# Kernel optimization log

Hardware: AMD Instinct MI355X
Metric: run time of the kernel (lower is better)

## Reference

```python
import jax, jax.numpy as jnp
import numpy as np

NUM_EMBEDDINGS = 1024
DIM = 256
COMMIT = 0.25


def setup_inputs() -> dict:
    key = jax.random.key(0)
    k_inp, k_emb = jax.random.split(key)
    inp = jax.random.normal(k_inp, (64, 1024, DIM), dtype=jnp.float32)
    # emb.weight.data.uniform_(-1/num_embeddings, 1/num_embeddings)
    emb = jax.random.uniform(
        k_emb, (NUM_EMBEDDINGS, DIM), dtype=jnp.float32,
        minval=-1.0 / NUM_EMBEDDINGS, maxval=1.0 / NUM_EMBEDDINGS)
    return {"inp": inp, "emb": emb}


def reference(inp, emb):
    flat = inp.reshape(-1, DIM)                       # [N, D]
    d = (jnp.sum(flat * flat, axis=1, keepdims=True)
         + jnp.sum(emb * emb, axis=1)
         - 2.0 * flat @ emb.T)
    idx = jnp.argmin(d, axis=1)                       # [N]
    # gather instead of one-hot matmul (same math)
    quant = emb[idx].reshape(inp.shape)               # [B, T, D]
    codebook_loss = jnp.mean((jax.lax.stop_gradient(quant) - inp) ** 2)
    commit_loss = jnp.mean((quant - jax.lax.stop_gradient(inp)) ** 2)
    loss = codebook_loss + COMMIT * commit_loss
    st = inp + jax.lax.stop_gradient(quant - inp)     # straight-through
    return st, loss, idx
```

## Files before the change

kernel.cpp:

```cpp
#include <hip/hip_runtime.h>
#include <math.h>

#define D 256
#define K 1024
#define NR 65536
#define ST_SIZE (NR * D)
#define LOSS_OFF ST_SIZE
#define IDX_OFF (ST_SIZE + 1)
#define BM 128
#define TPB 512
#define NRND 32
#define NBLK (NR / BM)
#define MARGIN 2e-3f
#define CAND_CAP 3072

typedef short bf16x8 __attribute__((ext_vector_type(8)));
typedef float f32x4 __attribute__((ext_vector_type(4)));

#define GLDS(g, s) __builtin_amdgcn_global_load_lds( \
    (const __attribute__((address_space(1))) unsigned int*)(g), \
    (__attribute__((address_space(3))) unsigned int*)(s), 16, 0, 0)

__device__ __forceinline__ unsigned f2bf(float f) {
    unsigned u = __float_as_uint(f);
    return (u + 0x7FFFu + ((u >> 16) & 1u)) >> 16;
}
__device__ __forceinline__ uint4 packB(float4 a, float4 b) {
    uint4 w;
    w.x = f2bf(-2.f * a.x) | (f2bf(-2.f * a.y) << 16);
    w.y = f2bf(-2.f * a.z) | (f2bf(-2.f * a.w) << 16);
    w.z = f2bf(-2.f * b.x) | (f2bf(-2.f * b.y) << 16);
    w.w = f2bf(-2.f * b.z) | (f2bf(-2.f * b.w) << 16);
    return w;
}

__device__ __forceinline__ float sq_nf(float x) {
    float s = x * x;
    asm volatile("" : "+v"(s));
    return s;
}
template <typename F>
__device__ __forceinline__ float np_sumsq256(F ld) {
    float tot[2];
    #pragma unroll
    for (int h = 0; h < 2; ++h) {
        const int base = h * 128;
        float r[8];
        #pragma unroll
        for (int j = 0; j < 8; ++j) r[j] = sq_nf(ld(base + j));
        for (int i = 8; i < 128; i += 8) {
            #pragma unroll
            for (int j = 0; j < 8; ++j) r[j] += sq_nf(ld(base + i + j));
        }
        tot[h] = ((r[0] + r[1]) + (r[2] + r[3])) + ((r[4] + r[5]) + (r[6] + r[7]));
    }
    return tot[0] + tot[1];
}

__global__ void prep_kernel(const float* __restrict__ emb,
                            unsigned short* __restrict__ pb,
                            float* __restrict__ se) {
    if (blockIdx.x < 128) {
        const int c  = blockIdx.x * 256 + threadIdx.x;
        const int ct = c >> 9;
        const int r  = c & 511;
        const int kb = r >> 6, l = r & 63;
        const float* srcp = emb + (size_t)(ct * 16 + (l & 15)) * D
                                + kb * 32 + (l >> 4) * 8;
        const float4* s4 = (const float4*)srcp;
        ((uint4*)pb)[c] = packB(s4[0], s4[1]);
    } else {
        const int k = (blockIdx.x - 128) * 256 + threadIdx.x;
        const float* row = emb + (size_t)k * D;
        se[k] = np_sumsq256([&](int i) { return row[i]; });
    }
}

__global__ __attribute__((amdgpu_waves_per_eu(2, 4))) __launch_bounds__(TPB)
void vq_main(const float* __restrict__ inp, const float* __restrict__ emb,
             const unsigned short* __restrict__ pb, const float* __restrict__ se,
             float* __restrict__ out, double* __restrict__ lsum) {
    __shared__ __align__(16) unsigned short Bt[2][8192];
    __shared__ float sx_s[BM];
    __shared__ float rfin[BM];
    __shared__ unsigned cand[CAND_CAP];
    __shared__ float candsc[CAND_CAP];
    __shared__ unsigned bestd[BM];
    __shared__ unsigned bestc[BM];
    __shared__ int ncand;

    const int t   = threadIdx.x;
    const int ws  = t >> 6;
    const int l   = t & 63;
    const int c16 = l & 15;
    const int g4  = l >> 4;
    const int r0  = blockIdx.x * BM;

    if (t < BM) { bestd[t] = 0xFFFFFFFFu; bestc[t] = 0xFFFFFFFFu; }
    if (t == 0) ncand = 0;

    bf16x8 afr[8];
    {
        const float* xrow = inp + (size_t)(r0 + ws * 16 + c16) * D;
        #pragma unroll
        for (int kb = 0; kb < 8; ++kb) {
            const float4* p4 = (const float4*)(xrow + kb * 32 + g4 * 8);
            float4 a = p4[0], b = p4[1];
            bf16x8 v;
            v[0] = (short)f2bf(a.x); v[1] = (short)f2bf(a.y);
            v[2] = (short)f2bf(a.z); v[3] = (short)f2bf(a.w);
            v[4] = (short)f2bf(b.x); v[5] = (short)f2bf(b.y);
            v[6] = (short)f2bf(b.z); v[7] = (short)f2bf(b.w);
            afr[kb] = v;
        }
    }

    {
        const int slot = t & 15, grp = t >> 4;
        const int j = slot & 7, h = slot >> 3;
        #pragma unroll
        for (int p = 0; p < 4; ++p) {
            const int row = p * 32 + grp;
            const float* base = inp + (size_t)(r0 + row) * D + h * 128 + j;
            float s = sq_nf(base[0]);
            #pragma unroll
            for (int i = 1; i < 16; ++i) s += sq_nf(base[i * 8]);
            #pragma unroll
            for (int m = 1; m <= 8; m <<= 1) s += __shfl_xor(s, m);
            if (slot == 0) sx_s[row] = s;
        }
    }

    float rmin[4];
    #pragma unroll
    for (int i = 0; i < 4; ++i) rmin[i] = INFINITY;

    const uint4* srcv = (const uint4*)pb;

    auto stage = [&](int buf, int cr) {
        const uint4* g = srcv + (size_t)cr * 1024;
        #pragma unroll
        for (int q = 0; q < 2; ++q) {
            char* lbase = (char*)&Bt[buf][0] + (q * 512 + ws * 64) * 16;
            GLDS(g + q * TPB + t, lbase);
        }
    };

    stage(0, 0);
    int cur = 0;
    for (int cr = 0; cr < NRND; ++cr) {
        __syncthreads();
        if (cr + 1 < NRND) stage(cur ^ 1, cr + 1);
        const bf16x8* bch = (const bf16x8*)&Bt[cur][0];
        f32x4 a0e, a0o, a1e, a1o;
        {
            const float sev0 = se[(cr * 2 + 0) * 16 + c16];
            const float sev1 = se[(cr * 2 + 1) * 16 + c16];
            #pragma unroll
            for (int i = 0; i < 4; ++i) { a0e[i] = sev0; a0o[i] = 0.f; a1e[i] = sev1; a1o[i] = 0.f; }
        }
        #pragma unroll
        for (int kb = 0; kb < 8; kb += 2) {
            a0e = __builtin_amdgcn_mfma_f32_16x16x32_bf16(afr[kb],     bch[kb * 64 + l],             a0e, 0, 0, 0);
            a1e = __builtin_amdgcn_mfma_f32_16x16x32_bf16(afr[kb],     bch[512 + kb * 64 + l],       a1e, 0, 0, 0);
            a0o = __builtin_amdgcn_mfma_f32_16x16x32_bf16(afr[kb + 1], bch[(kb + 1) * 64 + l],       a0o, 0, 0, 0);
            a1o = __builtin_amdgcn_mfma_f32_16x16x32_bf16(afr[kb + 1], bch[512 + (kb + 1) * 64 + l], a1o, 0, 0, 0);
        }
        float sc0[4], sc1[4];
        #pragma unroll
        for (int i = 0; i < 4; ++i) { sc0[i] = a0e[i] + a0o[i]; sc1[i] = a1e[i] + a1o[i]; }

        #pragma unroll
        for (int i = 0; i < 4; ++i) rmin[i] = fminf(rmin[i], fminf(sc0[i], sc1[i]));
        if ((cr & 1) == 0) {
            #pragma unroll
            for (int i = 0; i < 4; ++i) {
                #pragma unroll
                for (int m = 1; m <= 8; m <<= 1)
                    rmin[i] = fminf(rmin[i], __shfl_xor(rmin[i], m));
            }
        }
        #pragma unroll
        for (int i = 0; i < 4; ++i) {
            const int row_local = ws * 16 + g4 * 4 + i;
            if (sc0[i] <= rmin[i] + MARGIN) {
                const int p = atomicAdd(&ncand, 1);
                if (p < CAND_CAP) {
                    cand[p]   = ((unsigned)row_local << 10) | (unsigned)((cr * 2) * 16 + c16);
                    candsc[p] = sc0[i];
                }
            }
            if (sc1[i] <= rmin[i] + MARGIN) {
                const int p = atomicAdd(&ncand, 1);
                if (p < CAND_CAP) {
                    cand[p]   = ((unsigned)row_local << 10) | (unsigned)((cr * 2 + 1) * 16 + c16);
                    candsc[p] = sc1[i];
                }
            }
        }
        cur ^= 1;
    }
    #pragma unroll
    for (int i = 0; i < 4; ++i) {
        #pragma unroll
        for (int m = 1; m <= 8; m <<= 1)
            rmin[i] = fminf(rmin[i], __shfl_xor(rmin[i], m));
    }
    if (c16 == 0) {
        #pragma unroll
        for (int i = 0; i < 4; ++i)
            rfin[ws * 16 + g4 * 4 + i] = rmin[i];
    }
    __syncthreads();

    int n = ncand; if (n > CAND_CAP) n = CAND_CAP;
    {
        const int qw = l >> 4, lq = l & 15;
        for (int ci = ws * 4 + qw; ci < n; ci += 32) {
            const unsigned uc = cand[ci];
            const int row_local = uc >> 10, code = uc & 1023;
            const float sc = candsc[ci];
            if (sc <= rfin[row_local] + MARGIN) {
                const float4* xp = (const float4*)(inp + (size_t)(r0 + row_local) * D) + lq * 4;
                const float4* ep = (const float4*)(emb + (size_t)code * D) + lq * 4;
                float p = 0.f;
                #pragma unroll
                for (int q = 0; q < 4; ++q) {
                    float4 x = xp[q], e = ep[q];
                    p = fmaf(x.x, e.x, p);
                    p = fmaf(x.y, e.y, p);
                    p = fmaf(x.z, e.z, p);
                    p = fmaf(x.w, e.w, p);
                }
                #pragma unroll
                for (int m = 1; m <= 8; m <<= 1) p += __shfl_xor(p, m);
                const float tv = sx_s[row_local] + se[code];
                const float d  = fmaf(-2.f, p, tv);
                if (lq == 0) {
                    candsc[ci] = d;
                    atomicMin(&bestd[row_local], __float_as_uint(d));
                }
            } else if (lq == 0) {
                candsc[ci] = INFINITY;
            }
        }
    }
    __syncthreads();
    for (int ci = t; ci < n; ci += TPB) {
        const unsigned uc = cand[ci];
        if (__float_as_uint(candsc[ci]) == bestd[uc >> 10])
            atomicMin(&bestc[uc >> 10], uc & 1023u);
    }
    __syncthreads();
    if (t < BM) out[IDX_OFF + r0 + t] = (float)bestc[t];

    {
        float4* out4 = (float4*)(out + (size_t)r0 * D);
        const float4* emb4 = (const float4*)emb;
        #pragma unroll
        for (int i = 0; i < (BM * D) / (4 * TPB); ++i) {
            const int e = i * TPB + t;
            out4[e] = emb4[((size_t)bestc[e >> 6] << 6) + (e & 63)];
        }
    }

    if (t < 64) {
        double s = (double)__uint_as_float(bestd[t]) + (double)__uint_as_float(bestd[t + 64]);
        #pragma unroll
        for (int m = 1; m < 64; m <<= 1) s += __shfl_xor(s, m);
        if (t == 0) lsum[blockIdx.x] = s;
    }
}

__global__ void fin_kernel(const double* __restrict__ lsum, float* __restrict__ out) {
    const int l = threadIdx.x;
    double s = 0.0;
    #pragma unroll
    for (int i = 0; i < NBLK / 64; ++i) s += lsum[l * (NBLK / 64) + i];
    #pragma unroll
    for (int m = 1; m < 64; m <<= 1) s += __shfl_xor(s, m);
    if (l == 0) out[LOSS_OFF] = (float)(1.25 * s / (double)ST_SIZE);
}

extern "C" void kernel_launch(void* const* d_in, const int* in_sizes, int n_in,
                              void* d_out, int out_size, void* d_ws, size_t ws_size,
                              hipStream_t stream) {
    const float* inp = (const float*)d_in[0];
    const float* emb = (const float*)d_in[1];
    float* out = (float*)d_out;
    unsigned short* pb = (unsigned short*)d_ws;
    float*  se_ws      = (float*)((char*)d_ws + 524288);
    double* lsum       = (double*)((char*)d_ws + 528384);

    prep_kernel<<<132, 256, 0, stream>>>(emb, pb, se_ws);
    vq_main<<<NBLK, TPB, 0, stream>>>(inp, emb, pb, se_ws, out, lsum);
    fin_kernel<<<1, 64, 0, stream>>>(lsum, out);
}
```

Measured before the change: 142.1 us.

## Double block size and split codebook halves across wave pairs per row group

Raises threads per block to 1024 so each 16-row group is handled by two waves that each scan half of the codebook, rather than one wave scanning all of it. Running minima per row are shared between the two waves through LDS atomicMin on order-preserving float keys, and that shared value is also used to prune candidates during the scan. The goal is more waves in flight to hide MFMA and LDS latency, and fewer candidate pushes. In exchange it adds atomics and barriers over more threads, and the larger block can raise register pressure or lower occupancy.

```diff
diff --git a/kernel.cpp b/kernel.cpp
--- a/kernel.cpp
+++ b/kernel.cpp
@@ -8,7 +8,7 @@
 #define LOSS_OFF ST_SIZE
 #define IDX_OFF (ST_SIZE + 1)
 #define BM 128
-#define TPB 512
+#define TPB 1024
 #define NRND 32
 #define NBLK (NR / BM)
 #define MARGIN 2e-3f
@@ -32,6 +32,15 @@
     w.z = f2bf(-2.f * b.x) | (f2bf(-2.f * b.y) << 16);
     w.w = f2bf(-2.f * b.z) | (f2bf(-2.f * b.w) << 16);
     return w;
+}
+
+__device__ __forceinline__ unsigned fkey(float f) {
+    unsigned b = __float_as_uint(f);
+    return (b & 0x80000000u) ? ~b : (b | 0x80000000u);
+}
+__device__ __forceinline__ float finv(unsigned u) {
+    unsigned b = (u & 0x80000000u) ? (u ^ 0x80000000u) : ~u;
+    return __uint_as_float(b);
 }
 
 __device__ __forceinline__ float sq_nf(float x) {
@@ -76,13 +85,13 @@
     }
 }
 
-__global__ __attribute__((amdgpu_waves_per_eu(2, 4))) __launch_bounds__(TPB)
+__global__ __attribute__((amdgpu_waves_per_eu(2, 8))) __launch_bounds__(TPB)
 void vq_main(const float* __restrict__ inp, const float* __restrict__ emb,
              const unsigned short* __restrict__ pb, const float* __restrict__ se,
              float* __restrict__ out, double* __restrict__ lsum) {
     __shared__ __align__(16) unsigned short Bt[2][8192];
     __shared__ float sx_s[BM];
-    __shared__ float rfin[BM];
+    __shared__ unsigned rminsh[BM];
     __shared__ unsigned cand[CAND_CAP];
     __shared__ float candsc[CAND_CAP];
     __shared__ unsigned bestd[BM];
@@ -94,14 +103,16 @@
     const int l   = t & 63;
     const int c16 = l & 15;
     const int g4  = l >> 4;
+    const int rg  = ws >> 1;
+    const int ch  = ws & 1;
     const int r0  = blockIdx.x * BM;
 
-    if (t < BM) { bestd[t] = 0xFFFFFFFFu; bestc[t] = 0xFFFFFFFFu; }
+    if (t < BM) { bestd[t] = 0xFFFFFFFFu; bestc[t] = 0xFFFFFFFFu; rminsh[t] = 0xFFFFFFFFu; }
     if (t == 0) ncand = 0;
 
     bf16x8 afr[8];
     {
-        const float* xrow = inp + (size_t)(r0 + ws * 16 + c16) * D;
+        const float* xrow = inp + (size_t)(r0 + rg * 16 + c16) * D;
         #pragma unroll
         for (int kb = 0; kb < 8; ++kb) {
             const float4* p4 = (const float4*)(xrow + kb * 32 + g4 * 8);
@@ -119,8 +130,8 @@
         const int slot = t & 15, grp = t >> 4;
         const int j = slot & 7, h = slot >> 3;
         #pragma unroll
-        for (int p = 0; p < 4; ++p) {
-            const int row = p * 32 + grp;
+        for (int p = 0; p < 2; ++p) {
+            const int row = p * 64 + grp;
             const float* base = inp + (size_t)(r0 + row) * D + h * 128 + j;
             float s = sq_nf(base[0]);
             #pragma unroll
@@ -138,12 +149,10 @@
     const uint4* srcv = (const uint4*)pb;
 
     auto stage = [&](int buf, int cr) {
-        const uint4* g = srcv + (size_t)cr * 1024;
-        #pragma unroll
-        for (int q = 0; q < 2; ++q) {
-            char* lbase = (char*)&Bt[buf][0] + (q * 512 + ws * 64) * 16;
-            GLDS(g + q * TPB + t, lbase);
-        }
+        const uint4* g = srcv + ((t < 512) ? ((size_t)cr * 512 + t)
+                                           : ((size_t)(32 + cr) * 512 + (t - 512)));
+        char* lbase = (char*)&Bt[buf][0] + ws * 1024;
+        GLDS(g, lbase);
     };
 
     stage(0, 0);
@@ -151,27 +160,25 @@
     for (int cr = 0; cr < NRND; ++cr) {
         __syncthreads();
         if (cr + 1 < NRND) stage(cur ^ 1, cr + 1);
-        const bf16x8* bch = (const bf16x8*)&Bt[cur][0];
-        f32x4 a0e, a0o, a1e, a1o;
+        const bf16x8* bch = (const bf16x8*)&Bt[cur][ch * 4096];
+        const int ct = ch * 32 + cr;
+        f32x4 aE, aO;
         {
-            const float sev0 = se[(cr * 2 + 0) * 16 + c16];
-            const float sev1 = se[(cr * 2 + 1) * 16 + c16];
-            #pragma unroll
-            for (int i = 0; i < 4; ++i) { a0e[i] = sev0; a0o[i] = 0.f; a1e[i] = sev1; a1o[i] = 0.f; }
+            const float sev = se[ct * 16 + c16];
+            #pragma unroll
+            for (int i = 0; i < 4; ++i) { aE[i] = sev; aO[i] = 0.f; }
         }
         #pragma unroll
         for (int kb = 0; kb < 8; kb += 2) {
-            a0e = __builtin_amdgcn_mfma_f32_16x16x32_bf16(afr[kb],     bch[kb * 64 + l],             a0e, 0, 0, 0);
-            a1e = __builtin_amdgcn_mfma_f32_16x16x32_bf16(afr[kb],     bch[512 + kb * 64 + l],       a1e, 0, 0, 0);
-            a0o = __builtin_amdgcn_mfma_f32_16x16x32_bf16(afr[kb + 1], bch[(kb + 1) * 64 + l],       a0o, 0, 0, 0);
-            a1o = __builtin_amdgcn_mfma_f32_16x16x32_bf16(afr[kb + 1], bch[512 + (kb + 1) * 64 + l], a1o, 0, 0, 0);
-        }
-        float sc0[4], sc1[4];
-        #pragma unroll
-        for (int i = 0; i < 4; ++i) { sc0[i] = a0e[i] + a0o[i]; sc1[i] = a1e[i] + a1o[i]; }
-
-        #pragma unroll
-        for (int i = 0; i < 4; ++i) rmin[i] = fminf(rmin[i], fminf(sc0[i], sc1[i]));
+            aE = __builtin_amdgcn_mfma_f32_16x16x32_bf16(afr[kb],     bch[kb * 64 + l],       aE, 0, 0, 0);
+            aO = __builtin_amdgcn_mfma_f32_16x16x32_bf16(afr[kb + 1], bch[(kb + 1) * 64 + l], aO, 0, 0, 0);
+        }
+        float sc[4];
+        #pragma unroll
+        for (int i = 0; i < 4; ++i) sc[i] = aE[i] + aO[i];
+
+        #pragma unroll
+        for (int i = 0; i < 4; ++i) rmin[i] = fminf(rmin[i], sc[i]);
         if ((cr & 1) == 0) {
             #pragma unroll
             for (int i = 0; i < 4; ++i) {
@@ -179,24 +186,23 @@
                 for (int m = 1; m <= 8; m <<= 1)
                     rmin[i] = fminf(rmin[i], __shfl_xor(rmin[i], m));
             }
+            if (c16 == 0) {
+                #pragma unroll
+                for (int i = 0; i < 4; ++i)
+                    atomicMin(&rminsh[rg * 16 + g4 * 4 + i], fkey(rmin[i]));
+            }
         }
         #pragma unroll
         for (int i = 0; i < 4; ++i) {
-            const int row_local = ws * 16 + g4 * 4 + i;
-            if (sc0[i] <= rmin[i] + MARGIN) {
+            const int row_local = rg * 16 + g4 * 4 + i;
+            const float thr = fminf(rmin[i], finv(rminsh[row_local])) + MARGIN;
+            if (sc[i] <= thr) {
                 const int p = atomicAdd(&ncand, 1);
                 if (p < CAND_CAP) {
-                    cand[p]   = ((unsigned)row_local << 10) | (unsigned)((cr * 2) * 16 + c16);
-                    candsc[p] = sc0[i];
+                    cand[p]   = ((unsigned)row_local << 10) | (unsigned)(ct * 16 + c16);
+                    candsc[p] = sc[i];
                 }
             }
-            if (sc1[i] <= rmin[i] + MARGIN) {
-                const int p = atomicAdd(&ncand, 1);
-                if (p < CAND_CAP) {
-                    cand[p]   = ((unsigned)row_local << 10) | (unsigned)((cr * 2 + 1) * 16 + c16);
-                    candsc[p] = sc1[i];
-                }
-            }
         }
         cur ^= 1;
     }
@@ -209,18 +215,18 @@
     if (c16 == 0) {
         #pragma unroll
         for (int i = 0; i < 4; ++i)
-            rfin[ws * 16 + g4 * 4 + i] = rmin[i];
+            atomicMin(&rminsh[rg * 16 + g4 * 4 + i], fkey(rmin[i]));
     }
     __syncthreads();
 
     int n = ncand; if (n > CAND_CAP) n = CAND_CAP;
     {
         const int qw = l >> 4, lq = l & 15;
-        for (int ci = ws * 4 + qw; ci < n; ci += 32) {
+        for (int ci = ws * 4 + qw; ci < n; ci += 64) {
             const unsigned uc = cand[ci];
             const int row_local = uc >> 10, code = uc & 1023;
             const float sc = candsc[ci];
-            if (sc <= rfin[row_local] + MARGIN) {
+            if (sc <= finv(rminsh[row_local]) + MARGIN) {
                 const float4* xp = (const float4*)(inp + (size_t)(r0 + row_local) * D) + lq * 4;
                 const float4* ep = (const float4*)(emb + (size_t)code * D) + lq * 4;
                 float p = 0.f;
```

Result: slower. 190.4 us (+34.0%).
